# Performance work log

Hardware: AMD Instinct MI355X
Metric: run time of the kernel (lower is better)

Reference implementation:

```python
import jax, jax.numpy as jnp
import numpy as np

E, T, D_IN, D_H = 8, 2048, 2048, 5632


def setup_inputs() -> dict:
    key = jax.random.key(0)
    kx, kg, kd, ku = jax.random.split(key, 4)
    scale = 0.02  # init_std-like scaling for weights
    return {
        "x": jax.random.normal(kx, (E, T, D_IN), dtype=jnp.float32),
        "gate_proj": jax.random.normal(kg, (E, D_IN, D_H), dtype=jnp.float32) * scale,
        "down_proj": jax.random.normal(kd, (E, D_IN, D_H), dtype=jnp.float32) * scale,
        "up_proj": jax.random.normal(ku, (E, D_H, D_IN), dtype=jnp.float32) * scale,
        "tokens_per_expert": T,
    }


def reference(x, gate_proj, down_proj, up_proj, tokens_per_expert):
    # ep_size=1: dispatch/combine are identity. Grouped SwiGLU per expert.
    # x: [E, T, d_in]; gate/down: [E, d_in, d_h]; up: [E, d_h, d_in]
    g = jnp.einsum('etd,edh->eth', x, gate_proj)
    u = jnp.einsum('etd,edh->eth', x, down_proj)
    h = jax.nn.silu(g) * u  # [E, T, d_h]
    out = jnp.einsum('eth,ehd->etd', h, up_proj)  # [E, T, d_in]
    return out
```

## Files before the change

kernel.cpp:

```cpp
#include <hip/hip_runtime.h>
#include <hip/hip_bf16.h>


#define NEXP 8
#define TT   2048
#define DIN  2048
#define DH   5632

using short8 = __attribute__((ext_vector_type(8))) short;
using f32x4  = __attribute__((ext_vector_type(4))) float;

static __device__ __forceinline__ float bf2f(unsigned short u) {
    return __uint_as_float(((unsigned int)u) << 16);
}
static __device__ __forceinline__ unsigned short f2bf(float f) {
    unsigned int i = __float_as_uint(f);
    return (unsigned short)((i + 0x7FFFu + ((i >> 16) & 1u)) >> 16);
}
static __device__ __forceinline__ void gld16(const void* g, void* l) {
    __builtin_amdgcn_global_load_lds(
        (const __attribute__((address_space(1))) void*)g,
        (__attribute__((address_space(3))) void*)l, 16, 0, 0);
}

__global__ __launch_bounds__(512, 2) void gemm_gu(
    const unsigned short* __restrict__ Xb,
    const unsigned short* __restrict__ Wgt,
    const unsigned short* __restrict__ Wdt,
    unsigned short* __restrict__ Hb)
{
    __shared__ __align__(16) unsigned short lds[65536];

    const int tid  = threadIdx.x;
    const int wave = tid >> 6, lane = tid & 63;
    const int l15 = lane & 15, l4 = lane >> 4;
    const int wr = wave >> 2, wc = wave & 3;

    const int orig = blockIdx.x;
    const int e    = orig & 7;
    const int w    = orig >> 3;
    const int r32  = w & 31;
    const int m0   = (r32 & 7) * 256;
    const int n0   = ((w >> 5) * 4 + (r32 >> 3)) * 128;

    const int K = DIN, NT = DIN >> 6;

    const unsigned short* Ae = Xb  + (size_t)e * TT * DIN;
    const unsigned short* Gp = Wgt + (size_t)e * DH * DIN + (size_t)n0 * K;
    const unsigned short* Dp = Wdt + (size_t)e * DH * DIN + (size_t)n0 * K;

    const int c0 = tid, c1 = 512 + tid;
    const int cs0 = c0 ^ ((c0 >> 3) & 7), cs1 = c1 ^ ((c1 >> 3) & 7);
    const int row0 = cs0 >> 3, col0 = (cs0 & 7) * 8;
    const int row1 = cs1 >> 3, col1 = (cs1 & 7) * 8;

    int ibA[4][2], ibB[2][2];
#pragma unroll
    for (int s = 0; s < 4; ++s)
#pragma unroll
        for (int ks = 0; ks < 2; ++ks) {
            const int r = wr * 64 + s * 16 + l15;
            ibA[s][ks] = (r * 128 + ks * 64 + l4 * 16) ^ ((r & 7) << 4);
        }
#pragma unroll
    for (int s = 0; s < 2; ++s)
#pragma unroll
        for (int ks = 0; ks < 2; ++ks) {
            const int r = wc * 32 + s * 16 + l15;
            ibB[s][ks] = (r * 128 + ks * 64 + l4 * 16) ^ ((r & 7) << 4);
        }

    f32x4 acc[8][4] = {};
    short8 Aq[4][2], Gq[2][2], Dq[2][2];

    auto stageA = [&](int ro, int kk, int slot) {
        gld16(Ae + (size_t)(m0 + ro + row0) * K + (kk + col0), &lds[slot * 8192 + wave * 512]);
        gld16(Ae + (size_t)(m0 + ro + row1) * K + (kk + col1), &lds[slot * 8192 + 4096 + wave * 512]);
    };
    auto stageW = [&](const unsigned short* p, int kk, int slot) {
        gld16(p + (size_t)row0 * K + (kk + col0), &lds[slot * 8192 + wave * 512]);
        gld16(p + (size_t)row1 * K + (kk + col1), &lds[slot * 8192 + 4096 + wave * 512]);
    };

    stageA(0, 0, 0);  stageW(Gp, 0, 1);  stageW(Dp, 0, 2);  stageA(128, 0, 3);
    stageA(0, 64, 4); stageW(Gp, 64, 5); stageW(Dp, 64, 6);
    asm volatile("s_waitcnt vmcnt(6)" ::: "memory");
    asm volatile("s_barrier" ::: "memory");

    const char* ldsc = (const char*)lds;
    for (int t = 0; t < NT; ++t) {
        const int sA0 = ((4 * t + 0) & 7) * 16384;
        const int sG  = ((4 * t + 1) & 7) * 16384;
        const int sD  = ((4 * t + 2) & 7) * 16384;
        const int sA1 = ((4 * t + 3) & 7) * 16384;

#pragma unroll
        for (int s = 0; s < 4; ++s) {
            Aq[s][0] = *(const short8*)(ldsc + sA0 + ibA[s][0]);
            Aq[s][1] = *(const short8*)(ldsc + sA0 + ibA[s][1]);
        }
#pragma unroll
        for (int s = 0; s < 2; ++s) {
            Gq[s][0] = *(const short8*)(ldsc + sG + ibB[s][0]);
            Gq[s][1] = *(const short8*)(ldsc + sG + ibB[s][1]);
        }
        if (t + 1 < NT) stageA(128, (t + 1) * 64, (4 * t + 7) & 7);
        asm volatile("s_barrier" ::: "memory");
        asm volatile("s_waitcnt lgkmcnt(0)" ::: "memory");
        __builtin_amdgcn_sched_barrier(0);
        __builtin_amdgcn_s_setprio(1);
#pragma unroll
        for (int m = 0; m < 4; ++m)
#pragma unroll
            for (int n = 0; n < 2; ++n) {
                acc[m][n] = __builtin_amdgcn_mfma_f32_16x16x32_bf16(Aq[m][0], Gq[n][0], acc[m][n], 0, 0, 0);
                acc[m][n] = __builtin_amdgcn_mfma_f32_16x16x32_bf16(Aq[m][1], Gq[n][1], acc[m][n], 0, 0, 0);
            }
        __builtin_amdgcn_s_setprio(0);
        asm volatile("s_barrier" ::: "memory");

#pragma unroll
        for (int s = 0; s < 2; ++s) {
            Dq[s][0] = *(const short8*)(ldsc + sD + ibB[s][0]);
            Dq[s][1] = *(const short8*)(ldsc + sD + ibB[s][1]);
        }
        if (t + 2 < NT) stageA(0, (t + 2) * 64, (4 * t + 8) & 7);
        asm volatile("s_barrier" ::: "memory");
        asm volatile("s_waitcnt lgkmcnt(0)" ::: "memory");
        __builtin_amdgcn_sched_barrier(0);
        __builtin_amdgcn_s_setprio(1);
#pragma unroll
        for (int m = 0; m < 4; ++m)
#pragma unroll
            for (int n = 0; n < 2; ++n) {
                acc[m][2 + n] = __builtin_amdgcn_mfma_f32_16x16x32_bf16(Aq[m][0], Dq[n][0], acc[m][2 + n], 0, 0, 0);
                acc[m][2 + n] = __builtin_amdgcn_mfma_f32_16x16x32_bf16(Aq[m][1], Dq[n][1], acc[m][2 + n], 0, 0, 0);
            }
        __builtin_amdgcn_s_setprio(0);
        asm volatile("s_barrier" ::: "memory");

#pragma unroll
        for (int s = 0; s < 4; ++s) {
            Aq[s][0] = *(const short8*)(ldsc + sA1 + ibA[s][0]);
            Aq[s][1] = *(const short8*)(ldsc + sA1 + ibA[s][1]);
        }
        if (t + 2 < NT) stageW(Gp, (t + 2) * 64, (4 * t + 9) & 7);
        asm volatile("s_barrier" ::: "memory");
        asm volatile("s_waitcnt lgkmcnt(0)" ::: "memory");
        __builtin_amdgcn_sched_barrier(0);
        __builtin_amdgcn_s_setprio(1);
#pragma unroll
        for (int m = 0; m < 4; ++m)
#pragma unroll
            for (int n = 0; n < 2; ++n) {
                acc[4 + m][2 + n] = __builtin_amdgcn_mfma_f32_16x16x32_bf16(Aq[m][0], Dq[n][0], acc[4 + m][2 + n], 0, 0, 0);
                acc[4 + m][2 + n] = __builtin_amdgcn_mfma_f32_16x16x32_bf16(Aq[m][1], Dq[n][1], acc[4 + m][2 + n], 0, 0, 0);
            }
        __builtin_amdgcn_s_setprio(0);
        asm volatile("s_barrier" ::: "memory");

        if (t + 2 < NT) stageW(Dp, (t + 2) * 64, (4 * t + 10) & 7);
        asm volatile("s_barrier" ::: "memory");
        __builtin_amdgcn_s_setprio(1);
#pragma unroll
        for (int m = 0; m < 4; ++m)
#pragma unroll
            for (int n = 0; n < 2; ++n) {
                acc[4 + m][n] = __builtin_amdgcn_mfma_f32_16x16x32_bf16(Aq[m][0], Gq[n][0], acc[4 + m][n], 0, 0, 0);
                acc[4 + m][n] = __builtin_amdgcn_mfma_f32_16x16x32_bf16(Aq[m][1], Gq[n][1], acc[4 + m][n], 0, 0, 0);
            }
        __builtin_amdgcn_s_setprio(0);
        if (t < NT - 2)       asm volatile("s_waitcnt vmcnt(6)" ::: "memory");
        else if (t == NT - 2) asm volatile("s_waitcnt vmcnt(0)" ::: "memory");
        asm volatile("s_barrier" ::: "memory");
    }

    unsigned short* He = Hb + (size_t)e * TT * DH;
#pragma unroll
    for (int fm = 0; fm < 8; ++fm) {
        const int row_b = m0 + (fm >> 2) * 128 + wr * 64 + (fm & 3) * 16 + l4 * 4;
#pragma unroll
        for (int nr = 0; nr < 2; ++nr) {
            const int col = n0 + wc * 32 + nr * 16 + l15;
#pragma unroll
            for (int j = 0; j < 4; ++j) {
                const float g = acc[fm][nr][j];
                const float u = acc[fm][2 + nr][j];
                const float h = g / (1.f + __expf(-g)) * u;
                He[(size_t)(row_b + j) * DH + col] = f2bf(h);
            }
        }
    }
}

__global__ __launch_bounds__(512, 2) void gemm_out(
    const unsigned short* __restrict__ Ab,
    const unsigned short* __restrict__ Btb,
    float* __restrict__ Cf)
{
    __shared__ __align__(16) unsigned short lds[65536];

    const int tid  = threadIdx.x;
    const int wave = tid >> 6, lane = tid & 63;
    const int l15 = lane & 15, l4 = lane >> 4;
    const int wr = wave >> 2, wc = wave & 3;

    const int orig = blockIdx.x;
    const int e    = orig & 7;
    const int w    = orig >> 3;
    const int r32  = w & 31;
    const int m0   = (r32 & 7) * 256;
    const int n0   = ((w >> 5) * 4 + (r32 >> 3)) * 256;

    const int M = TT, N = DIN, K = DH, NT = K >> 6;
    const unsigned short* Ae = Ab  + (size_t)e * TT * DH;
    const unsigned short* Be = Btb + (size_t)e * DIN * DH;

    const int c0 = tid, c1 = 512 + tid;
    const int cs0 = c0 ^ ((c0 >> 3) & 7), cs1 = c1 ^ ((c1 >> 3) & 7);
    const int row0 = cs0 >> 3, col0 = (cs0 & 7) * 8;
    const int row1 = cs1 >> 3, col1 = (cs1 & 7) * 8;

    int ibA[4][2], ibB[2][2];
#pragma unroll
    for (int s = 0; s < 4; ++s)
#pragma unroll
        for (int ks = 0; ks < 2; ++ks) {
            const int r = wr * 64 + s * 16 + l15;
            ibA[s][ks] = (r * 128 + ks * 64 + l4 * 16) ^ ((r & 7) << 4);
        }
#pragma unroll
    for (int s = 0; s < 2; ++s)
#pragma unroll
        for (int ks = 0; ks < 2; ++ks) {
            const int r = wc * 32 + s * 16 + l15;
            ibB[s][ks] = (r * 128 + ks * 64 + l4 * 16) ^ ((r & 7) << 4);
        }

    f32x4 acc[8][4] = {};
    short8 Aq[4][2], B0q[2][2], B1q[2][2];

    auto stageA = [&](int ro, int kk, int slot) {
        gld16(Ae + (size_t)(m0 + ro + row0) * K + (kk + col0), &lds[slot * 8192 + wave * 512]);
        gld16(Ae + (size_t)(m0 + ro + row1) * K + (kk + col1), &lds[slot * 8192 + 4096 + wave * 512]);
    };
    auto stageB = [&](int co, int kk, int slot) {
        gld16(Be + (size_t)(n0 + co + row0) * K + (kk + col0), &lds[slot * 8192 + wave * 512]);
        gld16(Be + (size_t)(n0 + co + row1) * K + (kk + col1), &lds[slot * 8192 + 4096 + wave * 512]);
    };

    stageA(0, 0, 0); stageB(0, 0, 1); stageB(128, 0, 2); stageA(128, 0, 3);
    stageA(0, 64, 4); stageB(0, 64, 5); stageB(128, 64, 6);
    asm volatile("s_waitcnt vmcnt(6)" ::: "memory");
    asm volatile("s_barrier" ::: "memory");

    const char* ldsc = (const char*)lds;
    for (int t = 0; t < NT; ++t) {
        const int sA0 = ((4 * t + 0) & 7) * 16384;
        const int sB0 = ((4 * t + 1) & 7) * 16384;
        const int sB1 = ((4 * t + 2) & 7) * 16384;
        const int sA1 = ((4 * t + 3) & 7) * 16384;

#pragma unroll
        for (int s = 0; s < 4; ++s) {
            Aq[s][0] = *(const short8*)(ldsc + sA0 + ibA[s][0]);
            Aq[s][1] = *(const short8*)(ldsc + sA0 + ibA[s][1]);
        }
#pragma unroll
        for (int s = 0; s < 2; ++s) {
            B0q[s][0] = *(const short8*)(ldsc + sB0 + ibB[s][0]);
            B0q[s][1] = *(const short8*)(ldsc + sB0 + ibB[s][1]);
        }
        if (t + 1 < NT) stageA(128, (t + 1) * 64, (4 * t + 7) & 7);
        asm volatile("s_barrier" ::: "memory");
        asm volatile("s_waitcnt lgkmcnt(0)" ::: "memory");
        __builtin_amdgcn_sched_barrier(0);
        __builtin_amdgcn_s_setprio(1);
#pragma unroll
        for (int m = 0; m < 4; ++m)
#pragma unroll
            for (int n = 0; n < 2; ++n) {
                acc[m][n] = __builtin_amdgcn_mfma_f32_16x16x32_bf16(Aq[m][0], B0q[n][0], acc[m][n], 0, 0, 0);
                acc[m][n] = __builtin_amdgcn_mfma_f32_16x16x32_bf16(Aq[m][1], B0q[n][1], acc[m][n], 0, 0, 0);
            }
        __builtin_amdgcn_s_setprio(0);
        asm volatile("s_barrier" ::: "memory");

#pragma unroll
        for (int s = 0; s < 2; ++s) {
            B1q[s][0] = *(const short8*)(ldsc + sB1 + ibB[s][0]);
            B1q[s][1] = *(const short8*)(ldsc + sB1 + ibB[s][1]);
        }
        if (t + 2 < NT) stageA(0, (t + 2) * 64, (4 * t + 8) & 7);
        asm volatile("s_barrier" ::: "memory");
        asm volatile("s_waitcnt lgkmcnt(0)" ::: "memory");
        __builtin_amdgcn_sched_barrier(0);
        __builtin_amdgcn_s_setprio(1);
#pragma unroll
        for (int m = 0; m < 4; ++m)
#pragma unroll
            for (int n = 0; n < 2; ++n) {
                acc[m][2 + n] = __builtin_amdgcn_mfma_f32_16x16x32_bf16(Aq[m][0], B1q[n][0], acc[m][2 + n], 0, 0, 0);
                acc[m][2 + n] = __builtin_amdgcn_mfma_f32_16x16x32_bf16(Aq[m][1], B1q[n][1], acc[m][2 + n], 0, 0, 0);
            }
        __builtin_amdgcn_s_setprio(0);
        asm volatile("s_barrier" ::: "memory");

#pragma unroll
        for (int s = 0; s < 4; ++s) {
            Aq[s][0] = *(const short8*)(ldsc + sA1 + ibA[s][0]);
            Aq[s][1] = *(const short8*)(ldsc + sA1 + ibA[s][1]);
        }
        if (t + 2 < NT) stageB(0, (t + 2) * 64, (4 * t + 9) & 7);
        asm volatile("s_barrier" ::: "memory");
        asm volatile("s_waitcnt lgkmcnt(0)" ::: "memory");
        __builtin_amdgcn_sched_barrier(0);
        __builtin_amdgcn_s_setprio(1);
#pragma unroll
        for (int m = 0; m < 4; ++m)
#pragma unroll
            for (int n = 0; n < 2; ++n) {
                acc[4 + m][2 + n] = __builtin_amdgcn_mfma_f32_16x16x32_bf16(Aq[m][0], B1q[n][0], acc[4 + m][2 + n], 0, 0, 0);
                acc[4 + m][2 + n] = __builtin_amdgcn_mfma_f32_16x16x32_bf16(Aq[m][1], B1q[n][1], acc[4 + m][2 + n], 0, 0, 0);
            }
        __builtin_amdgcn_s_setprio(0);
        asm volatile("s_barrier" ::: "memory");

        if (t + 2 < NT) stageB(128, (t + 2) * 64, (4 * t + 10) & 7);
        asm volatile("s_barrier" ::: "memory");
        __builtin_amdgcn_s_setprio(1);
#pragma unroll
        for (int m = 0; m < 4; ++m)
#pragma unroll
            for (int n = 0; n < 2; ++n) {
                acc[4 + m][n] = __builtin_amdgcn_mfma_f32_16x16x32_bf16(Aq[m][0], B0q[n][0], acc[4 + m][n], 0, 0, 0);
                acc[4 + m][n] = __builtin_amdgcn_mfma_f32_16x16x32_bf16(Aq[m][1], B0q[n][1], acc[4 + m][n], 0, 0, 0);
            }
        __builtin_amdgcn_s_setprio(0);
        if (t < NT - 2)       asm volatile("s_waitcnt vmcnt(6)" ::: "memory");
        else if (t == NT - 2) asm volatile("s_waitcnt vmcnt(0)" ::: "memory");
        asm volatile("s_barrier" ::: "memory");
    }

    float* Ce = Cf + (size_t)e * TT * DIN;
#pragma unroll
    for (int fm = 0; fm < 8; ++fm) {
        const int row_b = (fm >> 2) * 128 + wr * 64 + (fm & 3) * 16 + l4 * 4;
#pragma unroll
        for (int fn = 0; fn < 4; ++fn) {
            const int col = n0 + (fn >> 1) * 128 + wc * 32 + (fn & 1) * 16 + l15;
#pragma unroll
            for (int j = 0; j < 4; ++j)
                Ce[(size_t)(m0 + row_b + j) * N + col] = acc[fm][fn][j];
        }
    }
}

__global__ __launch_bounds__(256) void transpose_f32_bf16(
    const float* __restrict__ in, unsigned short* __restrict__ out,
    int R, int C, size_t ies, size_t oes)
{
    in  += (size_t)blockIdx.z * ies;
    out += (size_t)blockIdx.z * oes;
    __shared__ unsigned short t[64][65];
    const int tid = threadIdx.x;
    const int lr = tid >> 4, lc = (tid & 15) * 4;
    const int r0 = blockIdx.y * 64, c0 = blockIdx.x * 64;
#pragma unroll
    for (int i = 0; i < 4; ++i) {
        const int row = lr + i * 16;
        const float4 v = *(const float4*)(in + (size_t)(r0 + row) * C + c0 + lc);
        t[row][lc + 0] = f2bf(v.x); t[row][lc + 1] = f2bf(v.y);
        t[row][lc + 2] = f2bf(v.z); t[row][lc + 3] = f2bf(v.w);
    }
    __syncthreads();
#pragma unroll
    for (int i = 0; i < 4; ++i) {
        const int crow = lr + i * 16;
        ushort4 wv;
        wv.x = t[lc + 0][crow]; wv.y = t[lc + 1][crow];
        wv.z = t[lc + 2][crow]; wv.w = t[lc + 3][crow];
        *(ushort4*)(out + (size_t)(c0 + crow) * R + r0 + lc) = wv;
    }
}

__global__ __launch_bounds__(256) void conv_f32_bf16(
    const float* __restrict__ in, unsigned short* __restrict__ out, int n4)
{
    int i = blockIdx.x * 256 + threadIdx.x;
    const int stride = gridDim.x * 256;
    for (; i < n4; i += stride) {
        const float4 v = ((const float4*)in)[i];
        ushort4 wv;
        wv.x = f2bf(v.x); wv.y = f2bf(v.y); wv.z = f2bf(v.z); wv.w = f2bf(v.w);
        ((ushort4*)out)[i] = wv;
    }
}

extern "C" void kernel_launch(void* const* d_in, const int* in_sizes, int n_in,
                              void* d_out, int out_size, void* d_ws, size_t ws_size,
                              hipStream_t stream)
{
    const float* x  = (const float*)d_in[0];
    const float* wg = (const float*)d_in[1];
    const float* wd = (const float*)d_in[2];
    const float* wu = (const float*)d_in[3];
    float* out = (float*)d_out;

    const size_t XSZ = (size_t)TT * DIN;
    const size_t WSZ = (size_t)DIN * DH;
    unsigned short* xb  = (unsigned short*)d_ws;
    unsigned short* wgt = xb  + (size_t)NEXP * XSZ;
    unsigned short* wdt = wgt + (size_t)NEXP * WSZ;
    unsigned short* hb  = wdt + (size_t)NEXP * WSZ;

    conv_f32_bf16<<<4096, 256, 0, stream>>>(x, xb, (int)(NEXP * XSZ / 4));
    transpose_f32_bf16<<<dim3(DH / 64, DIN / 64, NEXP), 256, 0, stream>>>(
        wg, wgt, DIN, DH, WSZ, WSZ);
    transpose_f32_bf16<<<dim3(DH / 64, DIN / 64, NEXP), 256, 0, stream>>>(
        wd, wdt, DIN, DH, WSZ, WSZ);
    gemm_gu<<<NEXP * (TT / 256) * (DH / 128), 512, 0, stream>>>(xb, wgt, wdt, hb);
    transpose_f32_bf16<<<dim3(DIN / 64, DH / 64, NEXP), 256, 0, stream>>>(
        wu, wgt, DH, DIN, WSZ, WSZ);
    gemm_out<<<NEXP * (TT / 256) * (DIN / 256), 512, 0, stream>>>(hb, wgt, out);
}
```

Baseline: 1.259 ms.

## Make both GEMMs persistent with 256 blocks looping over output tiles

Both GEMM kernels switch from one block per output tile to a persistent grid of 256 blocks, one per CU. Each block walks several N tiles in sequence, and the software pipeline carries over tile boundaries so the prefetch of the next tile's weights overlaps the current epilogue. This targets tail-wave imbalance and the pipeline ramp cost paid at every block launch. The tile-to-block mapping is now fixed and static, and the epilogue stores still stall the pipeline between tiles.

```diff
diff --git a/kernel.cpp b/kernel.cpp
--- a/kernel.cpp
+++ b/kernel.cpp
@@ -36,18 +36,18 @@
     const int l15 = lane & 15, l4 = lane >> 4;
     const int wr = wave >> 2, wc = wave & 3;
 
-    const int orig = blockIdx.x;
-    const int e    = orig & 7;
-    const int w    = orig >> 3;
-    const int r32  = w & 31;
-    const int m0   = (r32 & 7) * 256;
-    const int n0   = ((w >> 5) * 4 + (r32 >> 3)) * 128;
-
-    const int K = DIN, NT = DIN >> 6;
+    const int bid = blockIdx.x;
+    const int e   = bid & 7;
+    const int cu  = bid >> 3;
+    const int m0  = (cu & 7) * 256;
+    const int nb  = cu >> 3;
+
+    const int K = DIN;
 
     const unsigned short* Ae = Xb  + (size_t)e * TT * DIN;
-    const unsigned short* Gp = Wgt + (size_t)e * DH * DIN + (size_t)n0 * K;
-    const unsigned short* Dp = Wdt + (size_t)e * DH * DIN + (size_t)n0 * K;
+    const unsigned short* Gbase = Wgt + (size_t)e * DH * DIN;
+    const unsigned short* Dbase = Wdt + (size_t)e * DH * DIN;
+    unsigned short* He = Hb + (size_t)e * TT * DH;
 
     const int c0 = tid, c1 = 512 + tid;
     const int cs0 = c0 ^ ((c0 >> 3) & 7), cs1 = c1 ^ ((c1 >> 3) & 7);
@@ -82,114 +82,133 @@
         gld16(p + (size_t)row1 * K + (kk + col1), &lds[slot * 8192 + 4096 + wave * 512]);
     };
 
-    stageA(0, 0, 0);  stageW(Gp, 0, 1);  stageW(Dp, 0, 2);  stageA(128, 0, 3);
-    stageA(0, 64, 4); stageW(Gp, 64, 5); stageW(Dp, 64, 6);
+    const size_t NSTEP = (size_t)512 * K;
+    const unsigned short* Gc = Gbase + (size_t)(nb * 128) * K;
+    const unsigned short* Dc = Dbase + (size_t)(nb * 128) * K;
+
+    stageA(0, 0, 0);  stageW(Gc, 0, 1);  stageW(Dc, 0, 2);  stageA(128, 0, 3);
+    stageA(0, 64, 4); stageW(Gc, 64, 5); stageW(Dc, 64, 6);
     asm volatile("s_waitcnt vmcnt(6)" ::: "memory");
     asm volatile("s_barrier" ::: "memory");
 
     const char* ldsc = (const char*)lds;
-    for (int t = 0; t < NT; ++t) {
-        const int sA0 = ((4 * t + 0) & 7) * 16384;
-        const int sG  = ((4 * t + 1) & 7) * 16384;
-        const int sD  = ((4 * t + 2) & 7) * 16384;
-        const int sA1 = ((4 * t + 3) & 7) * 16384;
-
-#pragma unroll
-        for (int s = 0; s < 4; ++s) {
-            Aq[s][0] = *(const short8*)(ldsc + sA0 + ibA[s][0]);
-            Aq[s][1] = *(const short8*)(ldsc + sA0 + ibA[s][1]);
-        }
-#pragma unroll
-        for (int s = 0; s < 2; ++s) {
-            Gq[s][0] = *(const short8*)(ldsc + sG + ibB[s][0]);
-            Gq[s][1] = *(const short8*)(ldsc + sG + ibB[s][1]);
-        }
-        if (t + 1 < NT) stageA(128, (t + 1) * 64, (4 * t + 7) & 7);
-        asm volatile("s_barrier" ::: "memory");
-        asm volatile("s_waitcnt lgkmcnt(0)" ::: "memory");
-        __builtin_amdgcn_sched_barrier(0);
-        __builtin_amdgcn_s_setprio(1);
-#pragma unroll
-        for (int m = 0; m < 4; ++m)
-#pragma unroll
-            for (int n = 0; n < 2; ++n) {
-                acc[m][n] = __builtin_amdgcn_mfma_f32_16x16x32_bf16(Aq[m][0], Gq[n][0], acc[m][n], 0, 0, 0);
-                acc[m][n] = __builtin_amdgcn_mfma_f32_16x16x32_bf16(Aq[m][1], Gq[n][1], acc[m][n], 0, 0, 0);
-            }
-        __builtin_amdgcn_s_setprio(0);
-        asm volatile("s_barrier" ::: "memory");
-
-#pragma unroll
-        for (int s = 0; s < 2; ++s) {
-            Dq[s][0] = *(const short8*)(ldsc + sD + ibB[s][0]);
-            Dq[s][1] = *(const short8*)(ldsc + sD + ibB[s][1]);
-        }
-        if (t + 2 < NT) stageA(0, (t + 2) * 64, (4 * t + 8) & 7);
-        asm volatile("s_barrier" ::: "memory");
-        asm volatile("s_waitcnt lgkmcnt(0)" ::: "memory");
-        __builtin_amdgcn_sched_barrier(0);
-        __builtin_amdgcn_s_setprio(1);
-#pragma unroll
-        for (int m = 0; m < 4; ++m)
-#pragma unroll
-            for (int n = 0; n < 2; ++n) {
-                acc[m][2 + n] = __builtin_amdgcn_mfma_f32_16x16x32_bf16(Aq[m][0], Dq[n][0], acc[m][2 + n], 0, 0, 0);
-                acc[m][2 + n] = __builtin_amdgcn_mfma_f32_16x16x32_bf16(Aq[m][1], Dq[n][1], acc[m][2 + n], 0, 0, 0);
-            }
-        __builtin_amdgcn_s_setprio(0);
-        asm volatile("s_barrier" ::: "memory");
-
-#pragma unroll
-        for (int s = 0; s < 4; ++s) {
-            Aq[s][0] = *(const short8*)(ldsc + sA1 + ibA[s][0]);
-            Aq[s][1] = *(const short8*)(ldsc + sA1 + ibA[s][1]);
-        }
-        if (t + 2 < NT) stageW(Gp, (t + 2) * 64, (4 * t + 9) & 7);
-        asm volatile("s_barrier" ::: "memory");
-        asm volatile("s_waitcnt lgkmcnt(0)" ::: "memory");
-        __builtin_amdgcn_sched_barrier(0);
-        __builtin_amdgcn_s_setprio(1);
-#pragma unroll
-        for (int m = 0; m < 4; ++m)
-#pragma unroll
-            for (int n = 0; n < 2; ++n) {
-                acc[4 + m][2 + n] = __builtin_amdgcn_mfma_f32_16x16x32_bf16(Aq[m][0], Dq[n][0], acc[4 + m][2 + n], 0, 0, 0);
-                acc[4 + m][2 + n] = __builtin_amdgcn_mfma_f32_16x16x32_bf16(Aq[m][1], Dq[n][1], acc[4 + m][2 + n], 0, 0, 0);
-            }
-        __builtin_amdgcn_s_setprio(0);
-        asm volatile("s_barrier" ::: "memory");
-
-        if (t + 2 < NT) stageW(Dp, (t + 2) * 64, (4 * t + 10) & 7);
-        asm volatile("s_barrier" ::: "memory");
-        __builtin_amdgcn_s_setprio(1);
-#pragma unroll
-        for (int m = 0; m < 4; ++m)
-#pragma unroll
-            for (int n = 0; n < 2; ++n) {
-                acc[4 + m][n] = __builtin_amdgcn_mfma_f32_16x16x32_bf16(Aq[m][0], Gq[n][0], acc[4 + m][n], 0, 0, 0);
-                acc[4 + m][n] = __builtin_amdgcn_mfma_f32_16x16x32_bf16(Aq[m][1], Gq[n][1], acc[4 + m][n], 0, 0, 0);
-            }
-        __builtin_amdgcn_s_setprio(0);
-        if (t < NT - 2)       asm volatile("s_waitcnt vmcnt(6)" ::: "memory");
-        else if (t == NT - 2) asm volatile("s_waitcnt vmcnt(0)" ::: "memory");
-        asm volatile("s_barrier" ::: "memory");
-    }
-
-    unsigned short* He = Hb + (size_t)e * TT * DH;
-#pragma unroll
-    for (int fm = 0; fm < 8; ++fm) {
-        const int row_b = m0 + (fm >> 2) * 128 + wr * 64 + (fm & 3) * 16 + l4 * 4;
-#pragma unroll
-        for (int nr = 0; nr < 2; ++nr) {
-            const int col = n0 + wc * 32 + nr * 16 + l15;
-#pragma unroll
-            for (int j = 0; j < 4; ++j) {
-                const float g = acc[fm][nr][j];
-                const float u = acc[fm][2 + nr][j];
-                const float h = g / (1.f + __expf(-g)) * u;
-                He[(size_t)(row_b + j) * DH + col] = f2bf(h);
-            }
-        }
+    for (int i = 0; i < 11; ++i) {
+        const unsigned short* Gn = Gc + NSTEP;
+        const unsigned short* Dn = Dc + NSTEP;
+        for (int t = 0; t < 32; ++t) {
+            const int g = (i << 5) + t;
+            const int sA0 = ((4 * g + 0) & 7) * 16384;
+            const int sG  = ((4 * g + 1) & 7) * 16384;
+            const int sD  = ((4 * g + 2) & 7) * 16384;
+            const int sA1 = ((4 * g + 3) & 7) * 16384;
+
+#pragma unroll
+            for (int s = 0; s < 4; ++s) {
+                Aq[s][0] = *(const short8*)(ldsc + sA0 + ibA[s][0]);
+                Aq[s][1] = *(const short8*)(ldsc + sA0 + ibA[s][1]);
+            }
+#pragma unroll
+            for (int s = 0; s < 2; ++s) {
+                Gq[s][0] = *(const short8*)(ldsc + sG + ibB[s][0]);
+                Gq[s][1] = *(const short8*)(ldsc + sG + ibB[s][1]);
+            }
+            if (i < 10 || t + 1 < 32)
+                stageA(128, ((t + 1) & 31) * 64, (4 * g + 7) & 7);
+            asm volatile("s_barrier" ::: "memory");
+            asm volatile("s_waitcnt lgkmcnt(0)" ::: "memory");
+            __builtin_amdgcn_sched_barrier(0);
+            __builtin_amdgcn_s_setprio(1);
+#pragma unroll
+            for (int m = 0; m < 4; ++m)
+#pragma unroll
+                for (int n = 0; n < 2; ++n) {
+                    acc[m][n] = __builtin_amdgcn_mfma_f32_16x16x32_bf16(Aq[m][0], Gq[n][0], acc[m][n], 0, 0, 0);
+                    acc[m][n] = __builtin_amdgcn_mfma_f32_16x16x32_bf16(Aq[m][1], Gq[n][1], acc[m][n], 0, 0, 0);
+                }
+            __builtin_amdgcn_s_setprio(0);
+            asm volatile("s_barrier" ::: "memory");
+
+#pragma unroll
+            for (int s = 0; s < 2; ++s) {
+                Dq[s][0] = *(const short8*)(ldsc + sD + ibB[s][0]);
+                Dq[s][1] = *(const short8*)(ldsc + sD + ibB[s][1]);
+            }
+            if (i < 10 || t + 2 < 32)
+                stageA(0, ((t + 2) & 31) * 64, (4 * g + 8) & 7);
+            asm volatile("s_barrier" ::: "memory");
+            asm volatile("s_waitcnt lgkmcnt(0)" ::: "memory");
+            __builtin_amdgcn_sched_barrier(0);
+            __builtin_amdgcn_s_setprio(1);
+#pragma unroll
+            for (int m = 0; m < 4; ++m)
+#pragma unroll
+                for (int n = 0; n < 2; ++n) {
+                    acc[m][2 + n] = __builtin_amdgcn_mfma_f32_16x16x32_bf16(Aq[m][0], Dq[n][0], acc[m][2 + n], 0, 0, 0);
+                    acc[m][2 + n] = __builtin_amdgcn_mfma_f32_16x16x32_bf16(Aq[m][1], Dq[n][1], acc[m][2 + n], 0, 0, 0);
+                }
+            __builtin_amdgcn_s_setprio(0);
+            asm volatile("s_barrier" ::: "memory");
+
+#pragma unroll
+            for (int s = 0; s < 4; ++s) {
+                Aq[s][0] = *(const short8*)(ldsc + sA1 + ibA[s][0]);
+                Aq[s][1] = *(const short8*)(ldsc + sA1 + ibA[s][1]);
+            }
+            if (i < 10 || t + 2 < 32)
+                stageW((t + 2 < 32) ? Gc : Gn, ((t + 2) & 31) * 64, (4 * g + 9) & 7);
+            asm volatile("s_barrier" ::: "memory");
+            asm volatile("s_waitcnt lgkmcnt(0)" ::: "memory");
+            __builtin_amdgcn_sched_barrier(0);
+            __builtin_amdgcn_s_setprio(1);
+#pragma unroll
+            for (int m = 0; m < 4; ++m)
+#pragma unroll
+                for (int n = 0; n < 2; ++n) {
+                    acc[4 + m][2 + n] = __builtin_amdgcn_mfma_f32_16x16x32_bf16(Aq[m][0], Dq[n][0], acc[4 + m][2 + n], 0, 0, 0);
+                    acc[4 + m][2 + n] = __builtin_amdgcn_mfma_f32_16x16x32_bf16(Aq[m][1], Dq[n][1], acc[4 + m][2 + n], 0, 0, 0);
+                }
+            __builtin_amdgcn_s_setprio(0);
+            asm volatile("s_barrier" ::: "memory");
+
+            if (i < 10 || t + 2 < 32)
+                stageW((t + 2 < 32) ? Dc : Dn, ((t + 2) & 31) * 64, (4 * g + 10) & 7);
+            asm volatile("s_barrier" ::: "memory");
+            __builtin_amdgcn_s_setprio(1);
+#pragma unroll
+            for (int m = 0; m < 4; ++m)
+#pragma unroll
+                for (int n = 0; n < 2; ++n) {
+                    acc[4 + m][n] = __builtin_amdgcn_mfma_f32_16x16x32_bf16(Aq[m][0], Gq[n][0], acc[4 + m][n], 0, 0, 0);
+                    acc[4 + m][n] = __builtin_amdgcn_mfma_f32_16x16x32_bf16(Aq[m][1], Gq[n][1], acc[4 + m][n], 0, 0, 0);
+                }
+            __builtin_amdgcn_s_setprio(0);
+            if (g < 350)       asm volatile("s_waitcnt vmcnt(6)" ::: "memory");
+            else if (g == 350) asm volatile("s_waitcnt vmcnt(0)" ::: "memory");
+            asm volatile("s_barrier" ::: "memory");
+        }
+
+        const int n0i = (4 * i + nb) * 128;
+#pragma unroll
+        for (int fm = 0; fm < 8; ++fm) {
+            const int row_b = m0 + (fm >> 2) * 128 + wr * 64 + (fm & 3) * 16 + l4 * 4;
+#pragma unroll
+            for (int nr = 0; nr < 2; ++nr) {
+                const int col = n0i + wc * 32 + nr * 16 + l15;
+#pragma unroll
+                for (int j = 0; j < 4; ++j) {
+                    const float gv = acc[fm][nr][j];
+                    const float uv = acc[fm][2 + nr][j];
+                    const float h = gv / (1.f + __expf(-gv)) * uv;
+                    He[(size_t)(row_b + j) * DH + col] = f2bf(h);
+                }
+            }
+        }
+#pragma unroll
+        for (int m = 0; m < 8; ++m)
+#pragma unroll
+            for (int n = 0; n < 4; ++n)
+                acc[m][n] = (f32x4){0.f, 0.f, 0.f, 0.f};
+        Gc = Gn; Dc = Dn;
     }
 }
 
@@ -205,16 +224,15 @@
     const int l15 = lane & 15, l4 = lane >> 4;
     const int wr = wave >> 2, wc = wave & 3;
 
-    const int orig = blockIdx.x;
-    const int e    = orig & 7;
-    const int w    = orig >> 3;
-    const int r32  = w & 31;
-    const int m0   = (r32 & 7) * 256;
-    const int n0   = ((w >> 5) * 4 + (r32 >> 3)) * 256;
-
-    const int M = TT, N = DIN, K = DH, NT = K >> 6;
+    const int bid = blockIdx.x;
+    const int e   = bid & 7;
+    const int cu  = bid >> 3;
+    const int m0  = (cu & 7) * 256;
+    const int nb  = cu >> 3;
+
+    const int N = DIN, K = DH, NT = K >> 6;
     const unsigned short* Ae = Ab  + (size_t)e * TT * DH;
-    const unsigned short* Be = Btb + (size_t)e * DIN * DH;
+    const unsigned short* Bbase = Btb + (size_t)e * DIN * DH;
 
     const int c0 = tid, c1 = 512 + tid;
     const int cs0 = c0 ^ ((c0 >> 3) & 7), cs1 = c1 ^ ((c1 >> 3) & 7);
@@ -244,115 +262,145 @@
         gld16(Ae + (size_t)(m0 + ro + row0) * K + (kk + col0), &lds[slot * 8192 + wave * 512]);
         gld16(Ae + (size_t)(m0 + ro + row1) * K + (kk + col1), &lds[slot * 8192 + 4096 + wave * 512]);
     };
-    auto stageB = [&](int co, int kk, int slot) {
-        gld16(Be + (size_t)(n0 + co + row0) * K + (kk + col0), &lds[slot * 8192 + wave * 512]);
-        gld16(Be + (size_t)(n0 + co + row1) * K + (kk + col1), &lds[slot * 8192 + 4096 + wave * 512]);
+    auto stageB = [&](const unsigned short* base, int co, int kk, int slot) {
+        gld16(base + (size_t)(co + row0) * K + (kk + col0), &lds[slot * 8192 + wave * 512]);
+        gld16(base + (size_t)(co + row1) * K + (kk + col1), &lds[slot * 8192 + 4096 + wave * 512]);
     };
 
-    stageA(0, 0, 0); stageB(0, 0, 1); stageB(128, 0, 2); stageA(128, 0, 3);
-    stageA(0, 64, 4); stageB(0, 64, 5); stageB(128, 64, 6);
+    const size_t NSTEP = (size_t)1024 * K;
+    const unsigned short* Bc = Bbase + (size_t)(nb * 256) * K;
+
+    stageA(0, 0, 0); stageB(Bc, 0, 0, 1); stageB(Bc, 128, 0, 2); stageA(128, 0, 3);
+    stageA(0, 64, 4); stageB(Bc, 0, 64, 5); stageB(Bc, 128, 64, 6);
     asm volatile("s_waitcnt vmcnt(6)" ::: "memory");
     asm volatile("s_barrier" ::: "memory");
 
     const char* ldsc = (const char*)lds;
-    for (int t = 0; t < NT; ++t) {
-        const int sA0 = ((4 * t + 0) & 7) * 16384;
-        const int sB0 = ((4 * t + 1) & 7) * 16384;
-        const int sB1 = ((4 * t + 2) & 7) * 16384;
-        const int sA1 = ((4 * t + 3) & 7) * 16384;
-
-#pragma unroll
-        for (int s = 0; s < 4; ++s) {
-            Aq[s][0] = *(const short8*)(ldsc + sA0 + ibA[s][0]);
-            Aq[s][1] = *(const short8*)(ldsc + sA0 + ibA[s][1]);
-        }
-#pragma unroll
-        for (int s = 0; s < 2; ++s) {
-            B0q[s][0] = *(const short8*)(ldsc + sB0 + ibB[s][0]);
-            B0q[s][1] = *(const short8*)(ldsc + sB0 + ibB[s][1]);
-        }
-        if (t + 1 < NT) stageA(128, (t + 1) * 64, (4 * t + 7) & 7);
-        asm volatile("s_barrier" ::: "memory");
-        asm volatile("s_waitcnt lgkmcnt(0)" ::: "memory");
-        __builtin_amdgcn_sched_barrier(0);
-        __builtin_amdgcn_s_setprio(1);
-#pragma unroll
-        for (int m = 0; m < 4; ++m)
-#pragma unroll
-            for (int n = 0; n < 2; ++n) {
-                acc[m][n] = __builtin_amdgcn_mfma_f32_16x16x32_bf16(Aq[m][0], B0q[n][0], acc[m][n], 0, 0, 0);
-                acc[m][n] = __builtin_amdgcn_mfma_f32_16x16x32_bf16(Aq[m][1], B0q[n][1], acc[m][n], 0, 0, 0);
-            }
-        __builtin_amdgcn_s_setprio(0);
-        asm volatile("s_barrier" ::: "memory");
-
-#pragma unroll
-        for (int s = 0; s < 2; ++s) {
-            B1q[s][0] = *(const short8*)(ldsc + sB1 + ibB[s][0]);
-            B1q[s][1] = *(const short8*)(ldsc + sB1 + ibB[s][1]);
-        }
-        if (t + 2 < NT) stageA(0, (t + 2) * 64, (4 * t + 8) & 7);
-        asm volatile("s_barrier" ::: "memory");
-        asm volatile("s_waitcnt lgkmcnt(0)" ::: "memory");
-        __builtin_amdgcn_sched_barrier(0);
-        __builtin_amdgcn_s_setprio(1);
-#pragma unroll
-        for (int m = 0; m < 4; ++m)
-#pragma unroll
-            for (int n = 0; n < 2; ++n) {
-                acc[m][2 + n] = __builtin_amdgcn_mfma_f32_16x16x32_bf16(Aq[m][0], B1q[n][0], acc[m][2 + n], 0, 0, 0);
-                acc[m][2 + n] = __builtin_amdgcn_mfma_f32_16x16x32_bf16(Aq[m][1], B1q[n][1], acc[m][2 + n], 0, 0, 0);
-            }
-        __builtin_amdgcn_s_setprio(0);
-        asm volatile("s_barrier" ::: "memory");
-
-#pragma unroll
-        for (int s = 0; s < 4; ++s) {
-            Aq[s][0] = *(const short8*)(ldsc + sA1 + ibA[s][0]);
-            Aq[s][1] = *(const short8*)(ldsc + sA1 + ibA[s][1]);
-        }
-        if (t + 2 < NT) stageB(0, (t + 2) * 64, (4 * t + 9) & 7);
-        asm volatile("s_barrier" ::: "memory");
-        asm volatile("s_waitcnt lgkmcnt(0)" ::: "memory");
-        __builtin_amdgcn_sched_barrier(0);
-        __builtin_amdgcn_s_setprio(1);
-#pragma unroll
-        for (int m = 0; m < 4; ++m)
-#pragma unroll
-            for (int n = 0; n < 2; ++n) {
-                acc[4 + m][2 + n] = __builtin_amdgcn_mfma_f32_16x16x32_bf16(Aq[m][0], B1q[n][0], acc[4 + m][2 + n], 0, 0, 0);
-                acc[4 + m][2 + n] = __builtin_amdgcn_mfma_f32_16x16x32_bf16(Aq[m][1], B1q[n][1], acc[4 + m][2 + n], 0, 0, 0);
-            }
-        __builtin_amdgcn_s_setprio(0);
-        asm volatile("s_barrier" ::: "memory");
-
-        if (t + 2 < NT) stageB(128, (t + 2) * 64, (4 * t + 10) & 7);
-        asm volatile("s_barrier" ::: "memory");
-        __builtin_amdgcn_s_setprio(1);
-#pragma unroll
-        for (int m = 0; m < 4; ++m)
-#pragma unroll
-            for (int n = 0; n < 2; ++n) {
-                acc[4 + m][n] = __builtin_amdgcn_mfma_f32_16x16x32_bf16(Aq[m][0], B0q[n][0], acc[4 + m][n], 0, 0, 0);
-                acc[4 + m][n] = __builtin_amdgcn_mfma_f32_16x16x32_bf16(Aq[m][1], B0q[n][1], acc[4 + m][n], 0, 0, 0);
-            }
-        __builtin_amdgcn_s_setprio(0);
-        if (t < NT - 2)       asm volatile("s_waitcnt vmcnt(6)" ::: "memory");
-        else if (t == NT - 2) asm volatile("s_waitcnt vmcnt(0)" ::: "memory");
-        asm volatile("s_barrier" ::: "memory");
-    }
-
-    float* Ce = Cf + (size_t)e * TT * DIN;
-#pragma unroll
-    for (int fm = 0; fm < 8; ++fm) {
-        const int row_b = (fm >> 2) * 128 + wr * 64 + (fm & 3) * 16 + l4 * 4;
-#pragma unroll
-        for (int fn = 0; fn < 4; ++fn) {
-            const int col = n0 + (fn >> 1) * 128 + wc * 32 + (fn & 1) * 16 + l15;
-#pragma unroll
-            for (int j = 0; j < 4; ++j)
-                Ce[(size_t)(m0 + row_b + j) * N + col] = acc[fm][fn][j];
-        }
+    for (int i = 0; i < 2; ++i) {
+        const unsigned short* Bn = Bc + NSTEP;
+        for (int t = 0; t < 88; ++t) {
+            const int g = i * 88 + t;
+            const int sA0 = ((4 * g + 0) & 7) * 16384;
+            const int sB0 = ((4 * g + 1) & 7) * 16384;
+            const int sB1 = ((4 * g + 2) & 7) * 16384;
+            const int sA1 = ((4 * g + 3) & 7) * 16384;
+
+#pragma unroll
+            for (int s = 0; s < 4; ++s) {
+                Aq[s][0] = *(const short8*)(ldsc + sA0 + ibA[s][0]);
+                Aq[s][1] = *(const short8*)(ldsc + sA0 + ibA[s][1]);
+            }
+#pragma unroll
+            for (int s = 0; s < 2; ++s) {
+                B0q[s][0] = *(const short8*)(ldsc + sB0 + ibB[s][0]);
+                B0q[s][1] = *(const short8*)(ldsc + sB0 + ibB[s][1]);
+            }
+            {
+                const int tt = t + 1;
+                if (i < 1 || tt < 88)
+                    stageA(128, (tt >= 88 ? tt - 88 : tt) * 64, (4 * g + 7) & 7);
+            }
+            asm volatile("s_barrier" ::: "memory");
+            asm volatile("s_waitcnt lgkmcnt(0)" ::: "memory");
+            __builtin_amdgcn_sched_barrier(0);
+            __builtin_amdgcn_s_setprio(1);
+#pragma unroll
+            for (int m = 0; m < 4; ++m)
+#pragma unroll
+                for (int n = 0; n < 2; ++n) {
+                    acc[m][n] = __builtin_amdgcn_mfma_f32_16x16x32_bf16(Aq[m][0], B0q[n][0], acc[m][n], 0, 0, 0);
+                    acc[m][n] = __builtin_amdgcn_mfma_f32_16x16x32_bf16(Aq[m][1], B0q[n][1], acc[m][n], 0, 0, 0);
+                }
+            __builtin_amdgcn_s_setprio(0);
+            asm volatile("s_barrier" ::: "memory");
+
+#pragma unroll
+            for (int s = 0; s < 2; ++s) {
+                B1q[s][0] = *(const short8*)(ldsc + sB1 + ibB[s][0]);
+                B1q[s][1] = *(const short8*)(ldsc + sB1 + ibB[s][1]);
+            }
+            {
+                const int tt = t + 2;
+                if (i < 1 || tt < 88)
+                    stageA(0, (tt >= 88 ? tt - 88 : tt) * 64, (4 * g + 8) & 7);
+            }
+            asm volatile("s_barrier" ::: "memory");
+            asm volatile("s_waitcnt lgkmcnt(0)" ::: "memory");
+            __builtin_amdgcn_sched_barrier(0);
+            __builtin_amdgcn_s_setprio(1);
+#pragma unroll
+            for (int m = 0; m < 4; ++m)
+#pragma unroll
+                for (int n = 0; n < 2; ++n) {
+                    acc[m][2 + n] = __builtin_amdgcn_mfma_f32_16x16x32_bf16(Aq[m][0], B1q[n][0], acc[m][2 + n], 0, 0, 0);
+                    acc[m][2 + n] = __builtin_amdgcn_mfma_f32_16x16x32_bf16(Aq[m][1], B1q[n][1], acc[m][2 + n], 0, 0, 0);
+                }
+            __builtin_amdgcn_s_setprio(0);
+            asm volatile("s_barrier" ::: "memory");
+
+#pragma unroll
+            for (int s = 0; s < 4; ++s) {
+                Aq[s][0] = *(const short8*)(ldsc + sA1 + ibA[s][0]);
+                Aq[s][1] = *(const short8*)(ldsc + sA1 + ibA[s][1]);
+            }
+            {
+                const int tt = t + 2;
+                if (i < 1 || tt < 88)
+                    stageB((tt >= 88 ? Bn : Bc), 0, (tt >= 88 ? tt - 88 : tt) * 64, (4 * g + 9) & 7);
+            }
+            asm volatile("s_barrier" ::: "memory");
+            asm volatile("s_waitcnt lgkmcnt(0)" ::: "memory");
+            __builtin_amdgcn_sched_barrier(0);
+            __builtin_amdgcn_s_setprio(1);
+#pragma unroll
+            for (int m = 0; m < 4; ++m)
+#pragma unroll
+                for (int n = 0; n < 2; ++n) {
+                    acc[4 + m][2 + n] = __builtin_amdgcn_mfma_f32_16x16x32_bf16(Aq[m][0], B1q[n][0], acc[4 + m][2 + n], 0, 0, 0);
+                    acc[4 + m][2 + n] = __builtin_amdgcn_mfma_f32_16x16x32_bf16(Aq[m][1], B1q[n][1], acc[4 + m][2 + n], 0, 0, 0);
+                }
+            __builtin_amdgcn_s_setprio(0);
+            asm volatile("s_barrier" ::: "memory");
+
+            {
+                const int tt = t + 2;
+                if (i < 1 || tt < 88)
+                    stageB((tt >= 88 ? Bn : Bc), 128, (tt >= 88 ? tt - 88 : tt) * 64, (4 * g + 10) & 7);
+            }
+            asm volatile("s_barrier" ::: "memory");
+            __builtin_amdgcn_s_setprio(1);
+#pragma unroll
+            for (int m = 0; m < 4; ++m)
+#pragma unroll
+                for (int n = 0; n < 2; ++n) {
+                    acc[4 + m][n] = __builtin_amdgcn_mfma_f32_16x16x32_bf16(Aq[m][0], B0q[n][0], acc[4 + m][n], 0, 0, 0);
+                    acc[4 + m][n] = __builtin_amdgcn_mfma_f32_16x16x32_bf16(Aq[m][1], B0q[n][1], acc[4 + m][n], 0, 0, 0);
+                }
+            __builtin_amdgcn_s_setprio(0);
+            if (g < 174)       asm volatile("s_waitcnt vmcnt(6)" ::: "memory");
+            else if (g == 174) asm volatile("s_waitcnt vmcnt(0)" ::: "memory");
+            asm volatile("s_barrier" ::: "memory");
+        }
+
+        const int n0i = (4 * i + nb) * 256;
+        float* Ce = Cf + (size_t)e * TT * DIN;
+#pragma unroll
+        for (int fm = 0; fm < 8; ++fm) {
+            const int row_b = (fm >> 2) * 128 + wr * 64 + (fm & 3) * 16 + l4 * 4;
+#pragma unroll
+            for (int fn = 0; fn < 4; ++fn) {
+                const int col = n0i + (fn >> 1) * 128 + wc * 32 + (fn & 1) * 16 + l15;
+#pragma unroll
+                for (int j = 0; j < 4; ++j)
+                    Ce[(size_t)(m0 + row_b + j) * N + col] = acc[fm][fn][j];
+            }
+        }
+#pragma unroll
+        for (int m = 0; m < 8; ++m)
+#pragma unroll
+            for (int n = 0; n < 4; ++n)
+                acc[m][n] = (f32x4){0.f, 0.f, 0.f, 0.f};
+        Bc = Bn;
     }
 }
 
@@ -419,8 +467,8 @@
         wg, wgt, DIN, DH, WSZ, WSZ);
     transpose_f32_bf16<<<dim3(DH / 64, DIN / 64, NEXP), 256, 0, stream>>>(
         wd, wdt, DIN, DH, WSZ, WSZ);
-    gemm_gu<<<NEXP * (TT / 256) * (DH / 128), 512, 0, stream>>>(xb, wgt, wdt, hb);
+    gemm_gu<<<256, 512, 0, stream>>>(xb, wgt, wdt, hb);
     transpose_f32_bf16<<<dim3(DIN / 64, DH / 64, NEXP), 256, 0, stream>>>(
         wu, wgt, DH, DIN, WSZ, WSZ);
-    gemm_out<<<NEXP * (TT / 256) * (DIN / 256), 512, 0, stream>>>(hb, wgt, out);
-}
+    gemm_out<<<256, 512, 0, stream>>>(hb, wgt, out);
+}
```

Result: slower. 1.297 ms (+3.1%).
